# Optimization experiments

Hardware: AMD Instinct MI355X
Metric: run time of the kernel (lower is better)

The kernel has to match this reference:

```python
import jax, jax.numpy as jnp
import numpy as np
from functools import partial

STEPS = 4096
STATE = 5


def setup_inputs() -> dict:
    key = jax.random.key(0)
    k1, k2, k3 = jax.random.split(key, 3)
    measurements = jax.random.normal(k1, (STEPS, 2), dtype=jnp.float32) * 5.0
    true_positions = jax.random.normal(k2, (STEPS, 2), dtype=jnp.float32) * 5.0
    # X0 = rand(5,1) with first two entries = initial measurement (0,0 by default)
    X0 = jax.random.uniform(k3, (STATE, 1), dtype=jnp.float32)
    X0 = X0.at[0, 0].set(0.0).at[1, 0].set(0.0)
    Qm = jnp.array([1e-4], dtype=jnp.float32)          # Q_multiplier parameter
    R = 10.0 * jnp.eye(2, dtype=jnp.float32)            # R parameter
    return {"measurements": measurements, "true_positions": true_positions,
            "X0": X0, "Qm": Qm, "R": R}


def _ekf_loss(measurements, true_positions, X0, Qm, R):
    I5 = jnp.eye(STATE, dtype=X0.dtype)
    P0 = 100.0 * I5
    q = Qm[0]

    def step(carry, z):
        X, P = carry
        # predict: F = I, f only adds heading rate to heading (X[3] += X[4]*dt)
        X = X.at[3, 0].add(X[4, 0])
        P = P + q * I5                     # F P F^T + Q, with F = I, Q = q*I
        # update: H selects rows 0,1
        Y = z[:, None] - X[:2]             # (2,1) innovation
        S = P[:2, :2] + R                  # (2,2)
        K = P[:, :2] @ jnp.linalg.inv(S)   # (5,2) gain
        X = X + K @ Y
        P = P - K @ P[:2, :]               # (I - K H) P
        # prediction one step ahead: f(X), take (x, y)
        Xp = X.at[3, 0].add(X[4, 0])
        return (X, P), Xp[:2, 0]

    _, preds = jax.lax.scan(step, (X0, P0), measurements)  # preds: (STEPS, 2)
    return jnp.mean((preds - true_positions) ** 2)


def reference(measurements, true_positions, X0, Qm, R):
    return _ekf_loss(measurements, true_positions, X0, Qm, R)
```

## Files before the change

### kernel.cpp

```cpp
#include <hip/hip_runtime.h>
#include <math.h>

#define STEPS 4096
#define BLOCK 512
#define PER_THREAD (STEPS / BLOCK)
#define NWAVES (BLOCK / 64)

__global__ __launch_bounds__(BLOCK) void ekf_loss_kernel(
    const float* __restrict__ meas,
    const float* __restrict__ truep,
    const float* __restrict__ X0,
    const float* __restrict__ Qm,
    const float* __restrict__ Rm,
    float* __restrict__ out)
{
    const int tid = threadIdx.x;
    const int base = tid * PER_THREAD;

    const double q  = (double)Qm[0];
    const double rx = (double)Rm[0];
    const double ry = (double)Rm[3];

    const double discx = sqrt(q * q + 4.0 * q * rx);
    const double fppx = 0.5 * (q + discx);
    const double fmmx = 0.5 * (q - discx);
    const double a0p = 100.0 + q;
    const double w0x = (a0p - fppx) / (a0p - fmmx);
    const double l2rx = log2((fmmx + rx) / (fppx + rx));
    const double discy = sqrt(q * q + 4.0 * q * ry);
    const double fppy = 0.5 * (q + discy);
    const double fmmy = 0.5 * (q - discy);
    const double w0y = (a0p - fppy) / (a0p - fmmy);
    const double l2ry = log2((fmmy + ry) / (fppy + ry));

    double mxs[PER_THREAD], mys[PER_THREAD], bxs[PER_THREAD], bys[PER_THREAD];
    double cmx = 1.0, cmy = 1.0, cbx = 0.0, cby = 0.0;
#pragma unroll
    for (int i = 0; i < PER_THREAD; ++i) {
        const int s = base + i;
        const double wx = w0x * exp2((double)s * l2rx);
        const double apx = (fppx - wx * fmmx) / (1.0 - wx);
        const double kx = apx / (apx + rx);
        const double wy = w0y * exp2((double)s * l2ry);
        const double apy = (fppy - wy * fmmy) / (1.0 - wy);
        const double ky = apy / (apy + ry);
        const double zx = (double)meas[2 * s + 0];
        const double zy = (double)meas[2 * s + 1];
        mxs[i] = 1.0 - kx;
        mys[i] = 1.0 - ky;
        bxs[i] = kx * zx;
        bys[i] = ky * zy;
        cbx = mxs[i] * cbx + bxs[i];
        cby = mys[i] * cby + bys[i];
        cmx = mxs[i] * cmx;
        cmy = mys[i] * cmy;
    }

    __shared__ double smx[BLOCK], smy[BLOCK], sbx[BLOCK], sby[BLOCK];
    smx[tid] = cmx; smy[tid] = cmy; sbx[tid] = cbx; sby[tid] = cby;
    __syncthreads();
    for (int off = 1; off < BLOCK; off <<= 1) {
        double pmx = 1.0, pmy = 1.0, pbx = 0.0, pby = 0.0;
        const bool has = (tid >= off);
        if (has) {
            pmx = smx[tid - off]; pmy = smy[tid - off];
            pbx = sbx[tid - off]; pby = sby[tid - off];
        }
        __syncthreads();
        if (has) {
            cbx = cmx * pbx + cbx;
            cby = cmy * pby + cby;
            cmx = cmx * pmx;
            cmy = cmy * pmy;
            smx[tid] = cmx; smy[tid] = cmy; sbx[tid] = cbx; sby[tid] = cby;
        }
        __syncthreads();
    }

    const double x0 = (double)X0[0];
    const double y0 = (double)X0[1];
    double px, py;
    if (tid == 0) { px = x0; py = y0; }
    else {
        px = smx[tid - 1] * x0 + sbx[tid - 1];
        py = smy[tid - 1] * y0 + sby[tid - 1];
    }

    double acc = 0.0;
#pragma unroll
    for (int i = 0; i < PER_THREAD; ++i) {
        const int s = base + i;
        px = mxs[i] * px + bxs[i];
        py = mys[i] * py + bys[i];
        const double dx = px - (double)truep[2 * s + 0];
        const double dy = py - (double)truep[2 * s + 1];
        acc += dx * dx + dy * dy;
    }

#pragma unroll
    for (int off = 32; off > 0; off >>= 1)
        acc += __shfl_down(acc, off, 64);
    __shared__ double wacc[NWAVES];
    if ((tid & 63) == 0) wacc[tid >> 6] = acc;
    __syncthreads();
    if (tid == 0) {
        double tot = 0.0;
#pragma unroll
        for (int w = 0; w < NWAVES; ++w) tot += wacc[w];
        out[0] = (float)(tot / (double)(2 * STEPS));
    }
}

extern "C" void kernel_launch(void* const* d_in, const int* in_sizes, int n_in,
                              void* d_out, int out_size, void* d_ws, size_t ws_size,
                              hipStream_t stream) {
    const float* meas  = (const float*)d_in[0];
    const float* truep = (const float*)d_in[1];
    const float* X0    = (const float*)d_in[2];
    const float* Qm    = (const float*)d_in[3];
    const float* Rm    = (const float*)d_in[4];
    float* out = (float*)d_out;
    ekf_loss_kernel<<<1, BLOCK, 0, stream>>>(meas, truep, X0, Qm, Rm, out);
}
```

Baseline: 66.79 us.

## Switch EKF scan to float, wave-shuffle scan, and vectorized float4 loads

Converts the per-step gain computation and the affine-recurrence scan from double to float, rewriting the gain formula so each step needs one reciprocal. Replaces the shared-memory Hillis-Steele block scan, which synchronised at every level, with an intra-wave __shfl_up scan plus a small per-wave carry combine. Measurements and targets are now read with float4 loads. The aim is to cut FP64 throughput cost, barrier latency and load count, at the risk of float precision loss in the long product chains and the log2/exp2 closed form.

```diff
diff --git a/kernel.cpp b/kernel.cpp
--- a/kernel.cpp
+++ b/kernel.cpp
@@ -4,6 +4,7 @@
 #define STEPS 4096
 #define BLOCK 512
 #define PER_THREAD (STEPS / BLOCK)
+#define HALF_PT (PER_THREAD / 2)
 #define NWAVES (BLOCK / 64)
 
 __global__ __launch_bounds__(BLOCK) void ekf_loss_kernel(
@@ -14,100 +15,129 @@
     const float* __restrict__ Rm,
     float* __restrict__ out)
 {
-    const int tid = threadIdx.x;
+    const int tid  = threadIdx.x;
+    const int lane = tid & 63;
+    const int wave = tid >> 6;
     const int base = tid * PER_THREAD;
 
     const double q  = (double)Qm[0];
     const double rx = (double)Rm[0];
     const double ry = (double)Rm[3];
+    const double a0p = 100.0 + q;
 
-    const double discx = sqrt(q * q + 4.0 * q * rx);
-    const double fppx = 0.5 * (q + discx);
-    const double fmmx = 0.5 * (q - discx);
-    const double a0p = 100.0 + q;
-    const double w0x = (a0p - fppx) / (a0p - fmmx);
-    const double l2rx = log2((fmmx + rx) / (fppx + rx));
-    const double discy = sqrt(q * q + 4.0 * q * ry);
-    const double fppy = 0.5 * (q + discy);
-    const double fmmy = 0.5 * (q - discy);
-    const double w0y = (a0p - fppy) / (a0p - fmmy);
-    const double l2ry = log2((fmmy + ry) / (fppy + ry));
+    const double discx = sqrt(q*q + 4.0*q*rx);
+    const double fppx_d = 0.5*(q + discx), fmmx_d = 0.5*(q - discx);
+    const float w0x  = (float)((a0p - fppx_d) / (a0p - fmmx_d));
+    const float l2rx = (float)log2((fmmx_d + rx) / (fppx_d + rx));
+    const float fppx = (float)fppx_d, fmmx = (float)fmmx_d;
+    const float frx  = (float)(fppx_d + rx), fmrx = (float)(fmmx_d + rx);
+    const float rxf  = (float)rx;
 
-    double mxs[PER_THREAD], mys[PER_THREAD], bxs[PER_THREAD], bys[PER_THREAD];
-    double cmx = 1.0, cmy = 1.0, cbx = 0.0, cby = 0.0;
+    const double discy = sqrt(q*q + 4.0*q*ry);
+    const double fppy_d = 0.5*(q + discy), fmmy_d = 0.5*(q - discy);
+    const float w0y  = (float)((a0p - fppy_d) / (a0p - fmmy_d));
+    const float l2ry = (float)log2((fmmy_d + ry) / (fppy_d + ry));
+    const float fppy = (float)fppy_d, fmmy = (float)fmmy_d;
+    const float fry  = (float)(fppy_d + ry), fmry = (float)(fmmy_d + ry);
+    const float ryf  = (float)ry;
+
+    const float4* mz4 = reinterpret_cast<const float4*>(meas);
+    float4 mv[HALF_PT];
+#pragma unroll
+    for (int j = 0; j < HALF_PT; ++j) mv[j] = mz4[tid * HALF_PT + j];
+
+    float mxs[PER_THREAD], mys[PER_THREAD], bxs[PER_THREAD], bys[PER_THREAD];
+    float cmx = 1.0f, cmy = 1.0f, cbx = 0.0f, cby = 0.0f;
 #pragma unroll
     for (int i = 0; i < PER_THREAD; ++i) {
         const int s = base + i;
-        const double wx = w0x * exp2((double)s * l2rx);
-        const double apx = (fppx - wx * fmmx) / (1.0 - wx);
-        const double kx = apx / (apx + rx);
-        const double wy = w0y * exp2((double)s * l2ry);
-        const double apy = (fppy - wy * fmmy) / (1.0 - wy);
-        const double ky = apy / (apy + ry);
-        const double zx = (double)meas[2 * s + 0];
-        const double zy = (double)meas[2 * s + 1];
-        mxs[i] = 1.0 - kx;
-        mys[i] = 1.0 - ky;
-        bxs[i] = kx * zx;
-        bys[i] = ky * zy;
-        cbx = mxs[i] * cbx + bxs[i];
-        cby = mys[i] * cby + bys[i];
-        cmx = mxs[i] * cmx;
-        cmy = mys[i] * cmy;
+        const float zx = (i & 1) ? mv[i >> 1].z : mv[i >> 1].x;
+        const float zy = (i & 1) ? mv[i >> 1].w : mv[i >> 1].y;
+
+        const float wx = w0x * exp2f((float)s * l2rx);
+        const float Dx = frx - wx * fmrx;
+        const float Nx = fppx - wx * fmmx;
+        const float iDx = 1.0f / Dx;
+        const float kx = Nx * iDx;
+        const float mx = rxf * (1.0f - wx) * iDx;
+
+        const float wy = w0y * exp2f((float)s * l2ry);
+        const float Dy = fry - wy * fmry;
+        const float Ny = fppy - wy * fmmy;
+        const float iDy = 1.0f / Dy;
+        const float ky = Ny * iDy;
+        const float my = ryf * (1.0f - wy) * iDy;
+
+        mxs[i] = mx; mys[i] = my;
+        bxs[i] = kx * zx; bys[i] = ky * zy;
+        cbx = mx * cbx + bxs[i];
+        cby = my * cby + bys[i];
+        cmx *= mx;
+        cmy *= my;
     }
 
-    __shared__ double smx[BLOCK], smy[BLOCK], sbx[BLOCK], sby[BLOCK];
-    smx[tid] = cmx; smy[tid] = cmy; sbx[tid] = cbx; sby[tid] = cby;
-    __syncthreads();
-    for (int off = 1; off < BLOCK; off <<= 1) {
-        double pmx = 1.0, pmy = 1.0, pbx = 0.0, pby = 0.0;
-        const bool has = (tid >= off);
-        if (has) {
-            pmx = smx[tid - off]; pmy = smy[tid - off];
-            pbx = sbx[tid - off]; pby = sby[tid - off];
-        }
-        __syncthreads();
-        if (has) {
+#pragma unroll
+    for (int d = 1; d < 64; d <<= 1) {
+        const float pmx = __shfl_up(cmx, d, 64);
+        const float pbx = __shfl_up(cbx, d, 64);
+        const float pmy = __shfl_up(cmy, d, 64);
+        const float pby = __shfl_up(cby, d, 64);
+        if (lane >= d) {
             cbx = cmx * pbx + cbx;
             cby = cmy * pby + cby;
-            cmx = cmx * pmx;
-            cmy = cmy * pmy;
-            smx[tid] = cmx; smy[tid] = cmy; sbx[tid] = cbx; sby[tid] = cby;
+            cmx *= pmx;
+            cmy *= pmy;
         }
-        __syncthreads();
     }
 
-    const double x0 = (double)X0[0];
-    const double y0 = (double)X0[1];
-    double px, py;
-    if (tid == 0) { px = x0; py = y0; }
-    else {
-        px = smx[tid - 1] * x0 + sbx[tid - 1];
-        py = smy[tid - 1] * y0 + sby[tid - 1];
+    __shared__ float wmx[NWAVES], wmy[NWAVES], wbx[NWAVES], wby[NWAVES];
+    if (lane == 63) { wmx[wave] = cmx; wmy[wave] = cmy; wbx[wave] = cbx; wby[wave] = cby; }
+    __syncthreads();
+
+    float lmx = __shfl_up(cmx, 1, 64), lbx = __shfl_up(cbx, 1, 64);
+    float lmy = __shfl_up(cmy, 1, 64), lby = __shfl_up(cby, 1, 64);
+    if (lane == 0) { lmx = 1.0f; lbx = 0.0f; lmy = 1.0f; lby = 0.0f; }
+    float gmx = 1.0f, gbx = 0.0f, gmy = 1.0f, gby = 0.0f;
+    for (int w = 0; w < wave; ++w) {
+        gbx = wmx[w] * gbx + wbx[w];
+        gby = wmy[w] * gby + wby[w];
+        gmx *= wmx[w];
+        gmy *= wmy[w];
     }
+    const float emx = lmx * gmx, ebx = lmx * gbx + lbx;
+    const float emy = lmy * gmy, eby = lmy * gby + lby;
 
-    double acc = 0.0;
+    const float x0 = X0[0], y0 = X0[1];
+    float px = emx * x0 + ebx;
+    float py = emy * y0 + eby;
+
+    const float4* tp4 = reinterpret_cast<const float4*>(truep);
+    float acc = 0.0f;
 #pragma unroll
-    for (int i = 0; i < PER_THREAD; ++i) {
-        const int s = base + i;
-        px = mxs[i] * px + bxs[i];
-        py = mys[i] * py + bys[i];
-        const double dx = px - (double)truep[2 * s + 0];
-        const double dy = py - (double)truep[2 * s + 1];
+    for (int j = 0; j < HALF_PT; ++j) {
+        const float4 tv = tp4[tid * HALF_PT + j];
+        const int i0 = 2 * j, i1 = 2 * j + 1;
+        px = mxs[i0] * px + bxs[i0];
+        py = mys[i0] * py + bys[i0];
+        float dx = px - tv.x, dy = py - tv.y;
+        acc += dx * dx + dy * dy;
+        px = mxs[i1] * px + bxs[i1];
+        py = mys[i1] * py + bys[i1];
+        dx = px - tv.z; dy = py - tv.w;
         acc += dx * dx + dy * dy;
     }
 
 #pragma unroll
     for (int off = 32; off > 0; off >>= 1)
         acc += __shfl_down(acc, off, 64);
-    __shared__ double wacc[NWAVES];
-    if ((tid & 63) == 0) wacc[tid >> 6] = acc;
+    __shared__ float wacc[NWAVES];
+    if (lane == 0) wacc[wave] = acc;
     __syncthreads();
     if (tid == 0) {
-        double tot = 0.0;
+        float tot = 0.0f;
 #pragma unroll
         for (int w = 0; w < NWAVES; ++w) tot += wacc[w];
-        out[0] = (float)(tot / (double)(2 * STEPS));
+        out[0] = tot / (float)(2 * STEPS);
     }
 }
 
```

Measured after the change: 62.73 us. 1.06x faster.
